# Kernel optimization log

Hardware: AMD Instinct MI355X
Metric: run time of the kernel (lower is better)

## Reference

```python
import jax, jax.numpy as jnp
import numpy as np
from jax import lax

WIN = 9          # window_size
EPS = 1e-08      # eps


def _box_filter(x):
    """Separable 3D box-mean filter (VALID), equivalent to conv3d with
    ones(WIN,WIN,WIN)/WIN**3. x: (B,1,D',H',W') padded volume."""
    for kshape in ((WIN, 1, 1), (1, WIN, 1), (1, 1, WIN)):
        k = jnp.ones((1, 1) + kshape, x.dtype) / WIN  # (O,I,kd,kh,kw)
        x = lax.conv_general_dilated(
            x, k, window_strides=(1, 1, 1), padding='VALID',
            dimension_numbers=('NCDHW', 'OIDHW', 'NCDHW'))
    return x


def setup_inputs() -> dict:
    key = jax.random.key(0)
    k1, k2 = jax.random.split(key)
    shape = (2, 1, 128, 128, 128)
    fixed = jax.random.uniform(k1, shape, dtype=jnp.float32)
    warped = jax.random.uniform(k2, shape, dtype=jnp.float32)
    return {"fixed": fixed, "warped": warped}


def reference(fixed, warped):
    pad = WIN // 2
    pw = [(0, 0), (0, 0), (pad, pad), (pad, pad), (pad, pad)]
    f = jnp.pad(fixed, pw, mode='reflect')
    w = jnp.pad(warped, pw, mode='reflect')

    mu_f = _box_filter(f)
    mu_w = _box_filter(w)

    sigma_f = jnp.maximum(_box_filter(f * f) - mu_f * mu_f, EPS)
    sigma_w = jnp.maximum(_box_filter(w * w) - mu_w * mu_w, EPS)
    sigma_fw = _box_filter(f * w) - mu_f * mu_w

    denom = jnp.maximum(jnp.sqrt(jnp.maximum(sigma_f * sigma_w, EPS * EPS)), EPS)
    lncc = jnp.clip(sigma_fw / denom, -10.0, 10.0)
    lncc = jnp.nan_to_num(lncc, nan=0.0, posinf=1.0, neginf=-1.0)
    return -jnp.mean(lncc)
```

## Files before the change

kernel.cpp:

```cpp
#include <hip/hip_runtime.h>
#include <math.h>


#define NVOX 4194304
#define SLICE 16384
#define S1 (65535.0f / 9.0f)
#define DQ3 ((float)(81.0 / 65535.0 / 729.0))

__device__ __forceinline__ int refl(int p) {
    return 127 - abs(abs(p) - 127);
}

__global__ __launch_bounds__(256)
void lncc_w_kernel(const float* __restrict__ f, const float* __restrict__ w,
                   unsigned short* __restrict__ wq) {
    const int gtid = blockIdx.x * 256 + threadIdx.x;
    const int wo  = gtid & 15;
    const int row = gtid >> 4;
    const int w0  = wo << 3;
    const int edge = (wo == 0) ? 1 : ((wo == 15) ? 2 : 0);
    const int jbc  = (edge == 1) ? 0 : ((edge == 2) ? 112 : (w0 - 4));

    const float* fr = f + (size_t)row * 128 + jbc;
    const float* wr = w + (size_t)row * 128 + jbc;
    float Lf[16], Lw[16];
#pragma unroll
    for (int t = 0; t < 4; ++t) {
        *(float4*)&Lf[4 * t] = *(const float4*)&fr[4 * t];
        *(float4*)&Lw[4 * t] = *(const float4*)&wr[4 * t];
    }
    float fv[16], wv[16];
    if (edge == 1) {
        const int pm[16] = {4,3,2,1,0,1,2,3,4,5,6,7,8,9,10,11};
#pragma unroll
        for (int t = 0; t < 16; ++t) { fv[t] = Lf[pm[t]]; wv[t] = Lw[pm[t]]; }
    } else if (edge == 2) {
        const int pm[16] = {4,5,6,7,8,9,10,11,12,13,14,15,14,13,12,11};
#pragma unroll
        for (int t = 0; t < 16; ++t) { fv[t] = Lf[pm[t]]; wv[t] = Lw[pm[t]]; }
    } else {
#pragma unroll
        for (int t = 0; t < 16; ++t) { fv[t] = Lf[t]; wv[t] = Lw[t]; }
    }

    unsigned int q[5][8];
    float sf = 0.f, sw = 0.f, sff = 0.f, sww = 0.f, sfw = 0.f;
#pragma unroll
    for (int t = 0; t < 9; ++t) {
        sf += fv[t]; sw += wv[t];
        sff = fmaf(fv[t], fv[t], sff);
        sww = fmaf(wv[t], wv[t], sww);
        sfw = fmaf(fv[t], wv[t], sfw);
    }
    q[0][0] = (unsigned short)fmaf(sf,  S1, 0.5f);
    q[1][0] = (unsigned short)fmaf(sw,  S1, 0.5f);
    q[2][0] = (unsigned short)fmaf(sff, S1, 0.5f);
    q[3][0] = (unsigned short)fmaf(sww, S1, 0.5f);
    q[4][0] = (unsigned short)fmaf(sfw, S1, 0.5f);
#pragma unroll
    for (int k = 1; k < 8; ++k) {
        float fe = fv[k + 8], fx = fv[k - 1];
        float we = wv[k + 8], wx = wv[k - 1];
        sf += fe - fx; sw += we - wx;
        sff = fmaf(fe, fe, sff); sff = fmaf(-fx, fx, sff);
        sww = fmaf(we, we, sww); sww = fmaf(-wx, wx, sww);
        sfw = fmaf(fe, we, sfw); sfw = fmaf(-fx, wx, sfw);
        q[0][k] = (unsigned short)fmaf(sf,  S1, 0.5f);
        q[1][k] = (unsigned short)fmaf(sw,  S1, 0.5f);
        q[2][k] = (unsigned short)fmaf(sff, S1, 0.5f);
        q[3][k] = (unsigned short)fmaf(sww, S1, 0.5f);
        q[4][k] = (unsigned short)fmaf(sfw, S1, 0.5f);
    }
#pragma unroll
    for (int c = 0; c < 5; ++c) {
        uint4 P;
        P.x = q[c][0] | (q[c][1] << 16);
        P.y = q[c][2] | (q[c][3] << 16);
        P.z = q[c][4] | (q[c][5] << 16);
        P.w = q[c][6] | (q[c][7] << 16);
        *(uint4*)&wq[(size_t)c * NVOX + (size_t)row * 128 + w0] = P;
    }
}

__global__ __launch_bounds__(256)
void lncc_h_kernel(const unsigned short* __restrict__ wq,
                   unsigned short* __restrict__ whq) {
    const int gtid = blockIdx.x * 256 + threadIdx.x;
    const int wp = gtid & 63;
    const int ho = (gtid >> 6) & 15;
    const int bd = gtid >> 10;
    const int h0 = ho << 3;

#pragma unroll 1
    for (int c = 0; c < 5; ++c) {
        const unsigned short* base = wq + (size_t)c * NVOX + (size_t)bd * SLICE;
        unsigned short* ob = whq + (size_t)c * NVOX + (size_t)bd * SLICE;
        unsigned int v0[16], v1[16];
#pragma unroll
        for (int r = 0; r < 16; ++r) {
            int hh = refl(h0 - 4 + r);
            unsigned int pr = *(const unsigned int*)&base[(size_t)hh * 128 + 2 * wp];
            v0[r] = pr & 0xffffu;
            v1[r] = pr >> 16;
        }
        unsigned int s0 = 0, s1 = 0;
#pragma unroll
        for (int r = 0; r < 9; ++r) { s0 += v0[r]; s1 += v1[r]; }
#pragma unroll
        for (int k = 0; k < 8; ++k) {
            if (k > 0) { s0 += v0[k + 8] - v0[k - 1]; s1 += v1[k + 8] - v1[k - 1]; }
            unsigned int a = (unsigned short)fmaf((float)s0, 1.0f / 9.0f, 0.5f);
            unsigned int b = (unsigned short)fmaf((float)s1, 1.0f / 9.0f, 0.5f);
            *(unsigned int*)&ob[(size_t)(h0 + k) * 128 + 2 * wp] = a | (b << 16);
        }
    }
}

__global__ __launch_bounds__(256)
void lncc_d_kernel(const unsigned short* __restrict__ buf,
                   float* __restrict__ partials) {
    const int gtid = blockIdx.x * 256 + threadIdx.x;
    const int wc = gtid & 127;
    const int h  = (gtid >> 7) & 127;
    const int dc = (gtid >> 14) & 15;
    const int b  = gtid >> 18;
    const int d0 = dc << 3;

    float s[5][8];
#pragma unroll
    for (int c = 0; c < 5; ++c) {
        const unsigned short* bc = buf + (size_t)c * NVOX
                                 + (size_t)b * (128 * SLICE)
                                 + (size_t)h * 128 + wc;
        float v[16];
#pragma unroll
        for (int t = 0; t < 16; ++t) {
            int d = refl(d0 - 4 + t);
            v[t] = (float)bc[(size_t)d * SLICE];
        }
        float acc = 0.f;
#pragma unroll
        for (int t = 0; t < 9; ++t) acc += v[t];
        s[c][0] = acc;
#pragma unroll
        for (int j = 1; j < 8; ++j) {
            acc += v[j + 8] - v[j - 1];
            s[c][j] = acc;
        }
    }

    float lsum = 0.f;
#pragma unroll
    for (int j = 0; j < 8; ++j) {
        float mf = s[0][j] * DQ3;
        float mw = s[1][j] * DQ3;
        float sgf = fmaxf(s[2][j] * DQ3 - mf * mf, 1e-8f);
        float sgw = fmaxf(s[3][j] * DQ3 - mw * mw, 1e-8f);
        float sfw = s[4][j] * DQ3 - mf * mw;
        float denom = fmaxf(sqrtf(fmaxf(sgf * sgw, 1e-16f)), 1e-8f);
        float l = sfw / denom;
        lsum += fminf(fmaxf(l, -10.f), 10.f);
    }

#pragma unroll
    for (int off = 32; off > 0; off >>= 1)
        lsum += __shfl_down(lsum, off, 64);
    __shared__ float red[4];
    int lane = threadIdx.x & 63, wid = threadIdx.x >> 6;
    if (lane == 0) red[wid] = lsum;
    __syncthreads();
    if (threadIdx.x == 0)
        partials[blockIdx.x] = red[0] + red[1] + red[2] + red[3];
}

__global__ __launch_bounds__(256)
void lncc_final_kernel(const float* __restrict__ partials, int n,
                       float* __restrict__ out) {
    __shared__ double rd[256];
    double acc = 0.0;
    for (int i = threadIdx.x; i < n; i += 256) acc += (double)partials[i];
    rd[threadIdx.x] = acc;
    __syncthreads();
    for (int s = 128; s > 0; s >>= 1) {
        if (threadIdx.x < s) rd[threadIdx.x] += rd[threadIdx.x + s];
        __syncthreads();
    }
    if (threadIdx.x == 0) out[0] = (float)(-rd[0] / (double)NVOX);
}

extern "C" void kernel_launch(void* const* d_in, const int* in_sizes, int n_in,
                              void* d_out, int out_size, void* d_ws, size_t ws_size,
                              hipStream_t stream) {
    const float* f = (const float*)d_in[0];
    const float* w = (const float*)d_in[1];
    float* out = (float*)d_out;

    unsigned short* wqb  = (unsigned short*)d_ws;
    unsigned short* whqb = wqb + (size_t)5 * NVOX;
    float* partials = (float*)((char*)d_ws + (size_t)20 * NVOX);

    lncc_w_kernel<<<2048, 256, 0, stream>>>(f, w, wqb);
    lncc_h_kernel<<<1024, 256, 0, stream>>>(wqb, whqb);
    lncc_d_kernel<<<2048, 256, 0, stream>>>(whqb, partials);
    lncc_final_kernel<<<1, 256, 0, stream>>>(partials, 2048, out);
}
```

Before: 45.68 us.

## Fuse W and H box-filter passes through shared memory per slice strip

Merges the W-direction and H-direction box-filter kernels into one kernel. Each block computes the W-pass for a 16-column strip across all 128 rows of a slice, stages the quantized sums in LDS, then runs the H-pass from LDS. This removes the write and re-read of the five intermediate 16-bit volumes in global memory and one kernel launch. In exchange it uses about 30KB of LDS per block, which can limit occupancy, and the H-pass now does a direct 9-tap sum per output instead of a sliding window.

```diff
diff --git a/kernel.cpp b/kernel.cpp
--- a/kernel.cpp
+++ b/kernel.cpp
@@ -12,106 +12,111 @@
 }
 
 __global__ __launch_bounds__(256)
-void lncc_w_kernel(const float* __restrict__ f, const float* __restrict__ w,
-                   unsigned short* __restrict__ wq) {
-    const int gtid = blockIdx.x * 256 + threadIdx.x;
-    const int wo  = gtid & 15;
-    const int row = gtid >> 4;
-    const int w0  = wo << 3;
-    const int edge = (wo == 0) ? 1 : ((wo == 15) ? 2 : 0);
-    const int jbc  = (edge == 1) ? 0 : ((edge == 2) ? 112 : (w0 - 4));
-
-    const float* fr = f + (size_t)row * 128 + jbc;
-    const float* wr = w + (size_t)row * 128 + jbc;
-    float Lf[16], Lw[16];
-#pragma unroll
-    for (int t = 0; t < 4; ++t) {
-        *(float4*)&Lf[4 * t] = *(const float4*)&fr[4 * t];
-        *(float4*)&Lw[4 * t] = *(const float4*)&wr[4 * t];
-    }
-    float fv[16], wv[16];
-    if (edge == 1) {
-        const int pm[16] = {4,3,2,1,0,1,2,3,4,5,6,7,8,9,10,11};
-#pragma unroll
-        for (int t = 0; t < 16; ++t) { fv[t] = Lf[pm[t]]; wv[t] = Lw[pm[t]]; }
-    } else if (edge == 2) {
-        const int pm[16] = {4,5,6,7,8,9,10,11,12,13,14,15,14,13,12,11};
-#pragma unroll
-        for (int t = 0; t < 16; ++t) { fv[t] = Lf[pm[t]]; wv[t] = Lw[pm[t]]; }
-    } else {
-#pragma unroll
-        for (int t = 0; t < 16; ++t) { fv[t] = Lf[t]; wv[t] = Lw[t]; }
-    }
-
-    unsigned int q[5][8];
-    float sf = 0.f, sw = 0.f, sff = 0.f, sww = 0.f, sfw = 0.f;
-#pragma unroll
-    for (int t = 0; t < 9; ++t) {
-        sf += fv[t]; sw += wv[t];
-        sff = fmaf(fv[t], fv[t], sff);
-        sww = fmaf(wv[t], wv[t], sww);
-        sfw = fmaf(fv[t], wv[t], sfw);
-    }
-    q[0][0] = (unsigned short)fmaf(sf,  S1, 0.5f);
-    q[1][0] = (unsigned short)fmaf(sw,  S1, 0.5f);
-    q[2][0] = (unsigned short)fmaf(sff, S1, 0.5f);
-    q[3][0] = (unsigned short)fmaf(sww, S1, 0.5f);
-    q[4][0] = (unsigned short)fmaf(sfw, S1, 0.5f);
-#pragma unroll
-    for (int k = 1; k < 8; ++k) {
-        float fe = fv[k + 8], fx = fv[k - 1];
-        float we = wv[k + 8], wx = wv[k - 1];
-        sf += fe - fx; sw += we - wx;
-        sff = fmaf(fe, fe, sff); sff = fmaf(-fx, fx, sff);
-        sww = fmaf(we, we, sww); sww = fmaf(-wx, wx, sww);
-        sfw = fmaf(fe, we, sfw); sfw = fmaf(-fx, wx, sfw);
-        q[0][k] = (unsigned short)fmaf(sf,  S1, 0.5f);
-        q[1][k] = (unsigned short)fmaf(sw,  S1, 0.5f);
-        q[2][k] = (unsigned short)fmaf(sff, S1, 0.5f);
-        q[3][k] = (unsigned short)fmaf(sww, S1, 0.5f);
-        q[4][k] = (unsigned short)fmaf(sfw, S1, 0.5f);
-    }
-#pragma unroll
-    for (int c = 0; c < 5; ++c) {
-        uint4 P;
-        P.x = q[c][0] | (q[c][1] << 16);
-        P.y = q[c][2] | (q[c][3] << 16);
-        P.z = q[c][4] | (q[c][5] << 16);
-        P.w = q[c][6] | (q[c][7] << 16);
-        *(uint4*)&wq[(size_t)c * NVOX + (size_t)row * 128 + w0] = P;
-    }
-}
-
-__global__ __launch_bounds__(256)
-void lncc_h_kernel(const unsigned short* __restrict__ wq,
+void lncc_wh_fused(const float* __restrict__ f, const float* __restrict__ w,
                    unsigned short* __restrict__ whq) {
-    const int gtid = blockIdx.x * 256 + threadIdx.x;
-    const int wp = gtid & 63;
-    const int ho = (gtid >> 6) & 15;
-    const int bd = gtid >> 10;
-    const int h0 = ho << 3;
-
-#pragma unroll 1
-    for (int c = 0; c < 5; ++c) {
-        const unsigned short* base = wq + (size_t)c * NVOX + (size_t)bd * SLICE;
-        unsigned short* ob = whq + (size_t)c * NVOX + (size_t)bd * SLICE;
-        unsigned int v0[16], v1[16];
-#pragma unroll
-        for (int r = 0; r < 16; ++r) {
-            int hh = refl(h0 - 4 + r);
-            unsigned int pr = *(const unsigned int*)&base[(size_t)hh * 128 + 2 * wp];
-            v0[r] = pr & 0xffffu;
-            v1[r] = pr >> 16;
-        }
-        unsigned int s0 = 0, s1 = 0;
-#pragma unroll
-        for (int r = 0; r < 9; ++r) { s0 += v0[r]; s1 += v1[r]; }
-#pragma unroll
-        for (int k = 0; k < 8; ++k) {
-            if (k > 0) { s0 += v0[k + 8] - v0[k - 1]; s1 += v1[k + 8] - v1[k - 1]; }
-            unsigned int a = (unsigned short)fmaf((float)s0, 1.0f / 9.0f, 0.5f);
-            unsigned int b = (unsigned short)fmaf((float)s1, 1.0f / 9.0f, 0.5f);
-            *(unsigned int*)&ob[(size_t)(h0 + k) * 128 + 2 * wp] = a | (b << 16);
+    const int bid   = blockIdx.x;
+    const int slice = bid >> 3;
+    const int wgi   = bid & 7;
+    const int tid   = threadIdx.x;
+    const int h     = tid >> 1;
+    const int sub   = tid & 1;
+    const int wo    = wgi * 2 + sub;
+    const int w0    = wo << 3;
+
+    __shared__ unsigned int ldsw[5][128][12];
+
+    {
+        const int edge = (wo == 0) ? 1 : ((wo == 15) ? 2 : 0);
+        const int jbc  = (edge == 1) ? 0 : ((edge == 2) ? 112 : (w0 - 4));
+        const float* fr = f + (size_t)slice * SLICE + h * 128 + jbc;
+        const float* wr = w + (size_t)slice * SLICE + h * 128 + jbc;
+
+        float Lf[16], Lw[16];
+#pragma unroll
+        for (int t = 0; t < 4; ++t) {
+            *(float4*)&Lf[4 * t] = *(const float4*)&fr[4 * t];
+            *(float4*)&Lw[4 * t] = *(const float4*)&wr[4 * t];
+        }
+        float fv[16], wv[16];
+        if (edge == 1) {
+            const int pm[16] = {4,3,2,1,0,1,2,3,4,5,6,7,8,9,10,11};
+#pragma unroll
+            for (int t = 0; t < 16; ++t) { fv[t] = Lf[pm[t]]; wv[t] = Lw[pm[t]]; }
+        } else if (edge == 2) {
+            const int pm[16] = {4,5,6,7,8,9,10,11,12,13,14,15,14,13,12,11};
+#pragma unroll
+            for (int t = 0; t < 16; ++t) { fv[t] = Lf[pm[t]]; wv[t] = Lw[pm[t]]; }
+        } else {
+#pragma unroll
+            for (int t = 0; t < 16; ++t) { fv[t] = Lf[t]; wv[t] = Lw[t]; }
+        }
+
+        unsigned int q[5][8];
+        float sf = 0.f, sw = 0.f, sff = 0.f, sww = 0.f, sfw = 0.f;
+#pragma unroll
+        for (int t = 0; t < 9; ++t) {
+            sf += fv[t]; sw += wv[t];
+            sff = fmaf(fv[t], fv[t], sff);
+            sww = fmaf(wv[t], wv[t], sww);
+            sfw = fmaf(fv[t], wv[t], sfw);
+        }
+        q[0][0] = (unsigned short)fmaf(sf,  S1, 0.5f);
+        q[1][0] = (unsigned short)fmaf(sw,  S1, 0.5f);
+        q[2][0] = (unsigned short)fmaf(sff, S1, 0.5f);
+        q[3][0] = (unsigned short)fmaf(sww, S1, 0.5f);
+        q[4][0] = (unsigned short)fmaf(sfw, S1, 0.5f);
+#pragma unroll
+        for (int k = 1; k < 8; ++k) {
+            float fe = fv[k + 8], fx = fv[k - 1];
+            float we = wv[k + 8], wx = wv[k - 1];
+            sf += fe - fx; sw += we - wx;
+            sff = fmaf(fe, fe, sff); sff = fmaf(-fx, fx, sff);
+            sww = fmaf(we, we, sww); sww = fmaf(-wx, wx, sww);
+            sfw = fmaf(fe, we, sfw); sfw = fmaf(-fx, wx, sfw);
+            q[0][k] = (unsigned short)fmaf(sf,  S1, 0.5f);
+            q[1][k] = (unsigned short)fmaf(sw,  S1, 0.5f);
+            q[2][k] = (unsigned short)fmaf(sff, S1, 0.5f);
+            q[3][k] = (unsigned short)fmaf(sww, S1, 0.5f);
+            q[4][k] = (unsigned short)fmaf(sfw, S1, 0.5f);
+        }
+#pragma unroll
+        for (int c = 0; c < 5; ++c) {
+            uint4 P;
+            P.x = q[c][0] | (q[c][1] << 16);
+            P.y = q[c][2] | (q[c][3] << 16);
+            P.z = q[c][4] | (q[c][5] << 16);
+            P.w = q[c][6] | (q[c][7] << 16);
+            *(uint4*)&ldsw[c][h][sub * 4] = P;
+        }
+    }
+    __syncthreads();
+
+    {
+        unsigned short* ob = whq + (size_t)slice * SLICE + h * 128 + w0;
+#pragma unroll
+        for (int c = 0; c < 5; ++c) {
+            unsigned int s[8];
+#pragma unroll
+            for (int j = 0; j < 8; ++j) s[j] = 0;
+#pragma unroll
+            for (int i = 0; i < 9; ++i) {
+                const int rr = refl(h - 4 + i);
+                uint4 P = *(const uint4*)&ldsw[c][rr][sub * 4];
+                s[0] += P.x & 0xffffu;  s[1] += P.x >> 16;
+                s[2] += P.y & 0xffffu;  s[3] += P.y >> 16;
+                s[4] += P.z & 0xffffu;  s[5] += P.z >> 16;
+                s[6] += P.w & 0xffffu;  s[7] += P.w >> 16;
+            }
+            unsigned int r[8];
+#pragma unroll
+            for (int j = 0; j < 8; ++j)
+                r[j] = (unsigned short)fmaf((float)s[j], 1.0f / 9.0f, 0.5f);
+            uint4 Q;
+            Q.x = r[0] | (r[1] << 16);
+            Q.y = r[2] | (r[3] << 16);
+            Q.z = r[4] | (r[5] << 16);
+            Q.w = r[6] | (r[7] << 16);
+            *(uint4*)&ob[(size_t)c * NVOX] = Q;
         }
     }
 }
@@ -195,12 +200,10 @@
     const float* w = (const float*)d_in[1];
     float* out = (float*)d_out;
 
-    unsigned short* wqb  = (unsigned short*)d_ws;
-    unsigned short* whqb = wqb + (size_t)5 * NVOX;
-    float* partials = (float*)((char*)d_ws + (size_t)20 * NVOX);
-
-    lncc_w_kernel<<<2048, 256, 0, stream>>>(f, w, wqb);
-    lncc_h_kernel<<<1024, 256, 0, stream>>>(wqb, whqb);
+    unsigned short* whqb = (unsigned short*)d_ws;
+    float* partials = (float*)((char*)d_ws + (size_t)10 * NVOX);
+
+    lncc_wh_fused<<<2048, 256, 0, stream>>>(f, w, whqb);
     lncc_d_kernel<<<2048, 256, 0, stream>>>(whqb, partials);
     lncc_final_kernel<<<1, 256, 0, stream>>>(partials, 2048, out);
 }
```

New measurement: 54.70 us. +19.7%, slower.
